# Optimization experiments

Measured on AMD Instinct MI355X. Metric: run time of the kernel, lower is better.

## Reference

```python
import jax, jax.numpy as jnp
import numpy as np

EPS = 1e-3  # eps in grad_pursuit_update_step


def _grad_pursuit(signal, dictionary, target_l0):
    """signal: [B, V], dictionary: [F, V] -> dense weights [B, F] (nonneg)."""
    B, V = signal.shape
    F = dictionary.shape[0]
    rows = jnp.arange(B)

    def step(weights, _):
        # residual = signal - weights @ D         [B, V]
        residual = signal - jnp.einsum('bf,fv->bv', weights, dictionary)
        # inner products with every atom          [B, F]
        inner = jnp.einsum('bv,fv->bf', residual, dictionary)
        idx = jnp.argmax(inner, axis=1)           # [B]
        selected = (weights != 0).at[rows, idx].set(True)
        grad = jnp.where(selected, inner, jnp.zeros((), signal.dtype))  # [B, F]
        c = jnp.einsum('bf,fv->bv', grad, dictionary)                   # [B, V]
        c_sq = jnp.sum(c * c, axis=-1)
        step_size = jnp.sum(c * residual, axis=-1) / jnp.maximum(c_sq, EPS)
        weights = jax.nn.relu(weights + step_size[:, None] * grad)
        return weights, None

    w0 = jnp.zeros((B, F), dtype=signal.dtype)
    weights, _ = jax.lax.scan(step, w0, None, length=target_l0)
    return weights


def _decode(indices, weights, dictionary):
    # embedding-bag sum: gather rows then weighted sum over k
    return jnp.einsum('bk,bkv->bv', weights, dictionary[indices])


def setup_inputs() -> dict:
    key = jax.random.key(0)
    k1, k2, k3, k4, k5 = jax.random.split(key, 5)
    B, D, F = 1024, 1024, 8192
    x = jax.random.normal(k1, (B, D), dtype=jnp.float32)
    y = jax.random.normal(k2, (B, D), dtype=jnp.float32)
    xs = jax.random.normal(k3, (F, D), dtype=jnp.float32)
    xs = xs / jnp.linalg.norm(xs, axis=-1, keepdims=True)  # module stores unit-norm atoms
    ys = jax.random.normal(k4, (F, D), dtype=jnp.float32)
    ys = ys / jnp.linalg.norm(jax.random.normal(k3, (F, D)), axis=-1, keepdims=True)
    mean_y = 0.1 * jax.random.normal(k5, (D,), dtype=jnp.float32)
    return {"x": x, "y": y, "xs": xs, "ys": ys, "mean_y": mean_y, "target_l0": 16}


def reference(x, y, xs, ys, mean_y, target_l0):
    # ITDA.forward with subtract_mean=False, skip_connection=False, fvu_loss=True
    dense = _grad_pursuit(x, xs, target_l0)               # [B, F]
    weights, indices = jax.lax.top_k(dense, target_l0)    # [B, k], [B, k]
    x_rec = _decode(indices, weights, xs)                  # [B, V]
    y_rec = _decode(indices, weights, ys)                  # [B, V]
    l2 = jnp.sum((y - y_rec) ** 2, axis=-1)                # [B]
    total_var = jnp.mean(jnp.sum((y - mean_y) ** 2, axis=-1))
    losses = l2 / total_var
    return weights, indices, x_rec, y_rec, losses
```

## Files before the change

kernel.cpp:

```cpp
#include <hip/hip_runtime.h>
#include <cstdint>
#include <cstddef>

#define B_N 1024
#define V_N 1024
#define F_N 8192
#define NSEL 16
#define NITER 16
#define EPSV 1e-3f
#define WINF 0.008f
#define CANDMAX 64

#define BM 64
#define BN 128
#define BK 32
#define NBN (F_N / BN)

typedef __attribute__((ext_vector_type(4))) float f32x4;
typedef __attribute__((ext_vector_type(8))) short bf16x8;
typedef unsigned short u16;

#define GLDS16(g, l) __builtin_amdgcn_global_load_lds((__attribute__((address_space(1))) void*)(g), (__attribute__((address_space(3))) void*)(l), 16, 0, 0)

__device__ __forceinline__ u16 f2bf(float f) {
  unsigned u = __float_as_uint(f);
  return (u16)((u + 0x7FFFu + ((u >> 16) & 1u)) >> 16);
}

__device__ __forceinline__ float block_sum256(float v, float* sbuf) {
#pragma unroll
  for (int o = 32; o > 0; o >>= 1) v += __shfl_down(v, o, 64);
  int lane = threadIdx.x & 63, wid = threadIdx.x >> 6;
  if (lane == 0) sbuf[wid] = v;
  __syncthreads();
  float r = sbuf[0] + sbuf[1] + sbuf[2] + sbuf[3];
  __syncthreads();
  return r;
}

__device__ __forceinline__ float block_max256(float v, float* sbuf) {
#pragma unroll
  for (int o = 32; o > 0; o >>= 1) v = fmaxf(v, __shfl_down(v, o, 64));
  int lane = threadIdx.x & 63, wid = threadIdx.x >> 6;
  if (lane == 0) sbuf[wid] = v;
  __syncthreads();
  float r = fmaxf(fmaxf(sbuf[0], sbuf[1]), fmaxf(sbuf[2], sbuf[3]));
  __syncthreads();
  return r;
}

__device__ __forceinline__ float seq_dot(const float* __restrict__ xrow,
                                         const float* __restrict__ sr) {
  float acc = 0.f;
  for (int k = 0; k < V_N; k += 4) {
    float4 xv = *(const float4*)(xrow + k);
    acc = __builtin_fmaf(xv.x, sr[k + 0], acc);
    acc = __builtin_fmaf(xv.y, sr[k + 1], acc);
    acc = __builtin_fmaf(xv.z, sr[k + 2], acc);
    acc = __builtin_fmaf(xv.w, sr[k + 3], acc);
  }
  return acc;
}

__global__ __launch_bounds__(256) void rowvar_kernel(const float* __restrict__ y,
                                                     const float* __restrict__ mean_y,
                                                     float* __restrict__ rowvar,
                                                     int* __restrict__ act_cnt) {
  int b = blockIdx.x, t = threadIdx.x;
  __shared__ float sred[4];
  float4 yv = *(const float4*)(y + (size_t)b * V_N + t * 4);
  float4 mv = *(const float4*)(mean_y + t * 4);
  float dx = yv.x - mv.x, dy = yv.y - mv.y, dz = yv.z - mv.z, dw = yv.w - mv.w;
  float p = dx * dx + dy * dy + dz * dz + dw * dw;
  float s = block_sum256(p, sred);
  if (t == 0) { rowvar[b] = s; act_cnt[b] = 0; }
}

__global__ __launch_bounds__(256) void reduce_var_kernel(const float* __restrict__ rowvar,
                                                         float* __restrict__ totvar) {
  __shared__ float sred[4];
  int t = threadIdx.x;
  float p = 0.f;
#pragma unroll
  for (int i = 0; i < 4; i++) p += rowvar[t * 4 + i];
  float s = block_sum256(p, sred);
  if (t == 0) totvar[0] = s / (float)B_N;
}

__global__ __launch_bounds__(256) void xh_kernel(const float* __restrict__ xs,
                                                 u16* __restrict__ Xh) {
  int b = blockIdx.x, t = threadIdx.x;
  float4 v = *(const float4*)(xs + (size_t)b * V_N + t * 4);
  u16* o = Xh + (size_t)b * V_N + t * 4;
  o[0] = f2bf(v.x); o[1] = f2bf(v.y); o[2] = f2bf(v.z); o[3] = f2bf(v.w);
}

__global__ __launch_bounds__(256) void init_kernel(const float* __restrict__ x,
                                                   float* __restrict__ R,
                                                   u16* __restrict__ Rh,
                                                   float* __restrict__ rn2) {
  int b = blockIdx.x, t = threadIdx.x;
  __shared__ float sred[4];
  float4 v = *(const float4*)(x + (size_t)b * V_N + t * 4);
  *(float4*)(R + (size_t)b * V_N + t * 4) = v;
  u16* o = Rh + (size_t)b * V_N + t * 4;
  o[0] = f2bf(v.x); o[1] = f2bf(v.y); o[2] = f2bf(v.z); o[3] = f2bf(v.w);
  float p = v.x * v.x + v.y * v.y + v.z * v.z + v.w * v.w;
  float s = block_sum256(p, sred);
  if (t == 0) rn2[b] = s;
}

__global__ __launch_bounds__(256) void gemm_scan_kernel(const u16* __restrict__ Rh,
                                                        const u16* __restrict__ Xh,
                                                        float* __restrict__ inner) {
  __shared__ u16 As[128 * 32];
  __shared__ u16 Bs[128 * 32];
  const int tid = threadIdx.x;
  const int w = tid >> 6, l = tid & 63;
  const int bn = blockIdx.x, bm = blockIdx.y;
  const int wr = w >> 1, wc = w & 1;
  const int lr = l & 15, lg = l >> 4;

  f32x4 acc[4][4];
#pragma unroll
  for (int m = 0; m < 4; m++)
#pragma unroll
    for (int n = 0; n < 4; n++) acc[m][n] = (f32x4){0.f, 0.f, 0.f, 0.f};

  const u16* Ab = Rh + (size_t)bm * 128 * V_N;
  const u16* Bb = Xh + (size_t)bn * 128 * V_N;
  const int srow = w * 16 + (l >> 2);
  const int scol = (l & 3) * 8;

  for (int k0 = 0; k0 < V_N; k0 += 32) {
#pragma unroll
    for (int i = 0; i < 2; i++) {
      GLDS16(Ab + (size_t)(i * 64 + srow) * V_N + k0 + scol, As + i * 2048 + w * 512);
      GLDS16(Bb + (size_t)(i * 64 + srow) * V_N + k0 + scol, Bs + i * 2048 + w * 512);
    }
    __syncthreads();
    bf16x8 af[4], bfr[4];
#pragma unroll
    for (int m = 0; m < 4; m++) af[m] = *(const bf16x8*)&As[(wr * 64 + m * 16 + lr) * 32 + lg * 8];
#pragma unroll
    for (int n = 0; n < 4; n++) bfr[n] = *(const bf16x8*)&Bs[(wc * 64 + n * 16 + lr) * 32 + lg * 8];
#pragma unroll
    for (int m = 0; m < 4; m++)
#pragma unroll
      for (int n = 0; n < 4; n++)
        acc[m][n] = __builtin_amdgcn_mfma_f32_16x16x32_bf16(af[m], bfr[n], acc[m][n], 0, 0, 0);
    __syncthreads();
  }

#pragma unroll
  for (int m = 0; m < 4; m++) {
    int gm = bm * 128 + wr * 64 + m * 16 + lg * 4;
#pragma unroll
    for (int n = 0; n < 4; n++) {
      int gn = bn * 128 + wc * 64 + n * 16 + lr;
#pragma unroll
      for (int j = 0; j < 4; j++)
        inner[(size_t)(gm + j) * F_N + gn] = acc[m][n][j];
    }
  }
}

__global__ __launch_bounds__(256) void scan_update_kernel(const float* __restrict__ x,
                                                          const float* __restrict__ xs,
                                                          const float* __restrict__ inner,
                                                          float* __restrict__ rn2,
                                                          int* __restrict__ act_ids,
                                                          float* __restrict__ act_w,
                                                          int* __restrict__ act_cnt,
                                                          float* __restrict__ R,
                                                          u16* __restrict__ Rh) {
  int b = blockIdx.x, t = threadIdx.x;
  __shared__ float sr[V_N];
  __shared__ float sred[4];
  __shared__ float smax[4];
  __shared__ int   scand[CANDMAX];
  __shared__ float scval[CANDMAX];
  __shared__ float sfv[256];
  __shared__ int   sfi[256];
  __shared__ int   scnt_c;
  __shared__ int   sbii;
  __shared__ float sg[NSEL + 2];
  __shared__ float sw[NSEL + 2];
  __shared__ int   sids[NSEL + 2];
  __shared__ int   ssel[NSEL + 2];
  __shared__ int   scnt;

  float4 rv = *(const float4*)(R + (size_t)b * V_N + t * 4);
  *(float4*)&sr[t * 4] = rv;
  if (t == 0) scnt_c = 0;
  __syncthreads();

  const float* irow = inner + (size_t)b * F_N;
  float mx = -1e30f;
#pragma unroll
  for (int i = 0; i < 8; i++) {
    float4 v = *(const float4*)&irow[i * 1024 + t * 4];
    mx = fmaxf(mx, fmaxf(fmaxf(v.x, v.y), fmaxf(v.z, v.w)));
  }
  float M = block_max256(mx, smax);
  float win = WINF * sqrtf(rn2[b]);
  float thr = M - win;

#pragma unroll
  for (int i = 0; i < 8; i++) {
    float4 v = *(const float4*)&irow[i * 1024 + t * 4];
    int base = i * 1024 + t * 4;
    if (v.x >= thr) { int p = atomicAdd(&scnt_c, 1); if (p < CANDMAX) scand[p] = base + 0; }
    if (v.y >= thr) { int p = atomicAdd(&scnt_c, 1); if (p < CANDMAX) scand[p] = base + 1; }
    if (v.z >= thr) { int p = atomicAdd(&scnt_c, 1); if (p < CANDMAX) scand[p] = base + 2; }
    if (v.w >= thr) { int p = atomicAdd(&scnt_c, 1); if (p < CANDMAX) scand[p] = base + 3; }
  }
  __syncthreads();
  int total = scnt_c;
  int nc = total < CANDMAX ? total : CANDMAX;

  if (total > CANDMAX) {
    float bv = -1e30f; int bi = 0x7fffffff;
    for (int f = t; f < F_N; f += 256) {
      float acc = seq_dot(xs + (size_t)f * V_N, sr);
      if (acc > bv) { bv = acc; bi = f; }
    }
    sfv[t] = bv; sfi[t] = bi;
    __syncthreads();
    if (t == 0) {
      float bbv = sfv[0]; int bbi = sfi[0];
      for (int c = 1; c < 256; c++) {
        float v = sfv[c]; int id = sfi[c];
        if (v > bbv || (v == bbv && id < bbi)) { bbv = v; bbi = id; }
      }
      sbii = bbi;
    }
  } else if (nc == 1) {
    if (t == 0) sbii = scand[0];
  } else {
    if (t < nc) scval[t] = seq_dot(xs + (size_t)scand[t] * V_N, sr);
    __syncthreads();
    if (t == 0) {
      float bv = scval[0]; int bi = scand[0];
      for (int c = 1; c < nc; c++) {
        float v = scval[c]; int id = scand[c];
        if (v > bv || (v == bv && id < bi)) { bv = v; bi = id; }
      }
      sbii = bi;
    }
  }
  __syncthreads();

  if (t == 0) {
    int bi = sbii;
    int cnt = act_cnt[b];
    for (int j = 0; j < cnt; j++) { sids[j] = act_ids[b * NSEL + j]; sw[j] = act_w[b * NSEL + j]; }
    int pos = -1;
    for (int j = 0; j < cnt; j++) if (sids[j] == bi) pos = j;
    if (pos < 0) { pos = cnt; sids[cnt] = bi; sw[cnt] = 0.f; cnt++; }
    for (int j = 0; j < cnt; j++) ssel[j] = (sw[j] != 0.f) || (j == pos) ? 1 : 0;
    scnt = cnt;
  }
  __syncthreads();
  int cnt = scnt;

  for (int j = 0; j < cnt; j++) {
    if (!ssel[j]) { if (t == 0) sg[j] = 0.f; continue; }
    const float* xr = xs + (size_t)sids[j] * V_N;
    float4 xv = *(const float4*)(xr + t * 4);
    float4 rl = *(const float4*)&sr[t * 4];
    float p = xv.x * rl.x + xv.y * rl.y + xv.z * rl.z + xv.w * rl.w;
    float s = block_sum256(p, sred);
    if (t == 0) sg[j] = s;
  }
  __syncthreads();

  float4 cv = {0.f, 0.f, 0.f, 0.f};
  for (int j = 0; j < cnt; j++) {
    if (ssel[j]) {
      float g = sg[j];
      const float* xr = xs + (size_t)sids[j] * V_N;
      float4 xv = *(const float4*)(xr + t * 4);
      cv.x += g * xv.x; cv.y += g * xv.y; cv.z += g * xv.z; cv.w += g * xv.w;
    }
  }
  float4 rl = *(const float4*)&sr[t * 4];
  float pcsq = cv.x * cv.x + cv.y * cv.y + cv.z * cv.z + cv.w * cv.w;
  float pcr  = cv.x * rl.x + cv.y * rl.y + cv.z * rl.z + cv.w * rl.w;
  float csq = block_sum256(pcsq, sred);
  float cr  = block_sum256(pcr, sred);

  if (t == 0) {
    float step = cr / fmaxf(csq, EPSV);
    for (int j = 0; j < cnt; j++)
      if (ssel[j]) sw[j] = fmaxf(sw[j] + step * sg[j], 0.f);
    for (int j = 0; j < cnt; j++) {
      act_ids[b * NSEL + j] = sids[j];
      act_w[b * NSEL + j] = sw[j];
    }
    act_cnt[b] = cnt;
  }
  __syncthreads();

  float4 r = *(const float4*)(x + (size_t)b * V_N + t * 4);
  for (int j = 0; j < cnt; j++) {
    float wv = sw[j];
    if (wv != 0.f) {
      const float* xr = xs + (size_t)sids[j] * V_N;
      float4 xv = *(const float4*)(xr + t * 4);
      r.x -= wv * xv.x; r.y -= wv * xv.y; r.z -= wv * xv.z; r.w -= wv * xv.w;
    }
  }
  *(float4*)(R + (size_t)b * V_N + t * 4) = r;
  u16* o = Rh + (size_t)b * V_N + t * 4;
  o[0] = f2bf(r.x); o[1] = f2bf(r.y); o[2] = f2bf(r.z); o[3] = f2bf(r.w);
  float p2 = r.x * r.x + r.y * r.y + r.z * r.z + r.w * r.w;
  float s2 = block_sum256(p2, sred);
  if (t == 0) rn2[b] = s2;
}

__global__ __launch_bounds__(256) void residual_kernel(const float* __restrict__ x,
                                                       const float* __restrict__ xs,
                                                       const int* __restrict__ act_ids,
                                                       const float* __restrict__ act_w,
                                                       const int* __restrict__ act_cnt,
                                                       float* __restrict__ R) {
  int b = blockIdx.x, t = threadIdx.x;
  float4 r = *(const float4*)(x + (size_t)b * V_N + t * 4);
  int cnt = act_cnt[b];
  for (int j = 0; j < cnt; j++) {
    float w = act_w[b * NSEL + j];
    if (w != 0.f) {
      const float* xr = xs + (size_t)act_ids[b * NSEL + j] * V_N;
      float4 xv = *(const float4*)(xr + t * 4);
      r.x -= w * xv.x; r.y -= w * xv.y; r.z -= w * xv.z; r.w -= w * xv.w;
    }
  }
  *(float4*)(R + (size_t)b * V_N + t * 4) = r;
}

__global__ __launch_bounds__(256) void gemm_argmax_kernel(const float* __restrict__ R,
                                                          const float* __restrict__ xs,
                                                          float* __restrict__ pval,
                                                          int* __restrict__ pidx) {
  __shared__ float sA[BK * 68];
  __shared__ float sB[BK * 132];
  __shared__ float sMv[64 * 33];
  __shared__ int   sMi[64 * 33];

  int tid = threadIdx.x;
  int bn = blockIdx.x, bm = blockIdx.y;
  float acc[8][4];
#pragma unroll
  for (int i = 0; i < 8; i++)
#pragma unroll
    for (int j = 0; j < 4; j++) acc[i][j] = 0.f;

  int r0 = (tid >> 5) << 3;
  int n0 = (tid & 31) << 2;
  const float* Rbase = R + (size_t)(bm * BM) * V_N;
  const float* Xbase = xs + (size_t)(bn * BN) * V_N;

  for (int k0 = 0; k0 < V_N; k0 += BK) {
    {
      int m = tid >> 2, kf = (tid & 3) * 4;
      float4 v = *(const float4*)(Rbase + (size_t)m * V_N + k0 + kf);
      sA[(kf + 0) * 68 + m] = v.x; sA[(kf + 1) * 68 + m] = v.y;
      sA[(kf + 2) * 68 + m] = v.z; sA[(kf + 3) * 68 + m] = v.w;
      float4 v2 = *(const float4*)(Rbase + (size_t)m * V_N + k0 + kf + 16);
      sA[(kf + 16) * 68 + m] = v2.x; sA[(kf + 17) * 68 + m] = v2.y;
      sA[(kf + 18) * 68 + m] = v2.z; sA[(kf + 19) * 68 + m] = v2.w;
    }
    {
      int nn = tid >> 3, kf = (tid & 7) * 4;
#pragma unroll
      for (int i = 0; i < 4; i++) {
        int n = nn + i * 32;
        float4 v = *(const float4*)(Xbase + (size_t)n * V_N + k0 + kf);
        sB[(kf + 0) * 132 + n] = v.x; sB[(kf + 1) * 132 + n] = v.y;
        sB[(kf + 2) * 132 + n] = v.z; sB[(kf + 3) * 132 + n] = v.w;
      }
    }
    __syncthreads();
#pragma unroll
    for (int k = 0; k < BK; k++) {
      float4 aL = *(float4*)&sA[k * 68 + r0];
      float4 aH = *(float4*)&sA[k * 68 + r0 + 4];
      float4 bv = *(float4*)&sB[k * 132 + n0];
      float a[8] = {aL.x, aL.y, aL.z, aL.w, aH.x, aH.y, aH.z, aH.w};
      float bb[4] = {bv.x, bv.y, bv.z, bv.w};
#pragma unroll
      for (int i = 0; i < 8; i++)
#pragma unroll
        for (int j = 0; j < 4; j++) acc[i][j] += a[i] * bb[j];
    }
    __syncthreads();
  }

#pragma unroll
  for (int i = 0; i < 8; i++) {
    float bvv = acc[i][0]; int bj = 0;
#pragma unroll
    for (int j = 1; j < 4; j++)
      if (acc[i][j] > bvv) { bvv = acc[i][j]; bj = j; }
    sMv[(r0 + i) * 33 + (tid & 31)] = bvv;
    sMi[(r0 + i) * 33 + (tid & 31)] = bn * BN + n0 + bj;
  }
  __syncthreads();
  if (tid < 64) {
    float bvv = sMv[tid * 33]; int bi = sMi[tid * 33];
    for (int c = 1; c < 32; c++) {
      float v = sMv[tid * 33 + c];
      if (v > bvv) { bvv = v; bi = sMi[tid * 33 + c]; }
    }
    pval[(size_t)(bm * BM + tid) * NBN + bn] = bvv;
    pidx[(size_t)(bm * BM + tid) * NBN + bn] = bi;
  }
}

__global__ __launch_bounds__(256) void combine_update_kernel(const float* __restrict__ R,
                                                             const float* __restrict__ xs,
                                                             const float* __restrict__ pval,
                                                             const int* __restrict__ pidx,
                                                             int* __restrict__ act_ids,
                                                             float* __restrict__ act_w,
                                                             int* __restrict__ act_cnt) {
  int b = blockIdx.x, t = threadIdx.x;
  __shared__ float sr[V_N];
  __shared__ float sred[4];
  __shared__ float sg[NSEL + 1];
  __shared__ float sw[NSEL + 1];
  __shared__ int   sids[NSEL + 1];
  __shared__ int   ssel[NSEL + 1];
  __shared__ int   scnt;

  float4 rv = *(const float4*)(R + (size_t)b * V_N + t * 4);
  *(float4*)&sr[t * 4] = rv;

  if (t == 0) {
    const float* pv = pval + (size_t)b * NBN;
    const int* pi = pidx + (size_t)b * NBN;
    float bv = pv[0]; int bi = pi[0];
    for (int c = 1; c < NBN; c++) {
      float v = pv[c];
      if (v > bv) { bv = v; bi = pi[c]; }
    }
    int cnt = act_cnt[b];
    for (int j = 0; j < cnt; j++) { sids[j] = act_ids[b * NSEL + j]; sw[j] = act_w[b * NSEL + j]; }
    int pos = -1;
    for (int j = 0; j < cnt; j++) if (sids[j] == bi) pos = j;
    if (pos < 0) { pos = cnt; sids[cnt] = bi; sw[cnt] = 0.f; cnt++; }
    for (int j = 0; j < cnt; j++) ssel[j] = (sw[j] != 0.f) || (j == pos) ? 1 : 0;
    scnt = cnt;
  }
  __syncthreads();
  int cnt = scnt;

  for (int j = 0; j < cnt; j++) {
    if (!ssel[j]) { if (t == 0) sg[j] = 0.f; continue; }
    const float* xr = xs + (size_t)sids[j] * V_N;
    float4 xv = *(const float4*)(xr + t * 4);
    float4 rl = *(const float4*)&sr[t * 4];
    float p = xv.x * rl.x + xv.y * rl.y + xv.z * rl.z + xv.w * rl.w;
    float s = block_sum256(p, sred);
    if (t == 0) sg[j] = s;
  }
  __syncthreads();

  float4 cv = {0.f, 0.f, 0.f, 0.f};
  for (int j = 0; j < cnt; j++) {
    if (ssel[j]) {
      float g = sg[j];
      const float* xr = xs + (size_t)sids[j] * V_N;
      float4 xv = *(const float4*)(xr + t * 4);
      cv.x += g * xv.x; cv.y += g * xv.y; cv.z += g * xv.z; cv.w += g * xv.w;
    }
  }
  float4 rl = *(const float4*)&sr[t * 4];
  float pcsq = cv.x * cv.x + cv.y * cv.y + cv.z * cv.z + cv.w * cv.w;
  float pcr  = cv.x * rl.x + cv.y * rl.y + cv.z * rl.z + cv.w * rl.w;
  float csq = block_sum256(pcsq, sred);
  float cr  = block_sum256(pcr, sred);

  if (t == 0) {
    float step = cr / fmaxf(csq, EPSV);
    for (int j = 0; j < cnt; j++)
      if (ssel[j]) sw[j] = fmaxf(sw[j] + step * sg[j], 0.f);
    for (int j = 0; j < cnt; j++) {
      act_ids[b * NSEL + j] = sids[j];
      act_w[b * NSEL + j] = sw[j];
    }
    act_cnt[b] = cnt;
  }
}

__global__ __launch_bounds__(256) void topk_kernel(const int* __restrict__ act_ids,
                                                   const float* __restrict__ act_w,
                                                   const int* __restrict__ act_cnt,
                                                   float* __restrict__ out_w,
                                                   float* __restrict__ out_i) {
  int b = blockIdx.x * blockDim.x + threadIdx.x;
  if (b >= B_N) return;
  int cnt = act_cnt[b];
  int ids[NSEL]; float w[NSEL]; int m = 0;
  for (int j = 0; j < cnt; j++) {
    float wv = act_w[b * NSEL + j];
    if (wv > 0.f) { ids[m] = act_ids[b * NSEL + j]; w[m] = wv; m++; }
  }
  for (int i = 1; i < m; i++) {
    float wv = w[i]; int id = ids[i]; int j = i - 1;
    while (j >= 0 && (w[j] < wv || (w[j] == wv && ids[j] > id))) {
      w[j + 1] = w[j]; ids[j + 1] = ids[j]; j--;
    }
    w[j + 1] = wv; ids[j + 1] = id;
  }
  int nf = 0;
  for (int s = m; s < NSEL; s++) {
    for (;;) {
      bool used = false;
      for (int j = 0; j < m; j++) if (ids[j] == nf) used = true;
      if (!used) break;
      nf++;
    }
    ids[s] = nf; w[s] = 0.f; nf++;
  }
  for (int s = 0; s < NSEL; s++) {
    out_w[b * NSEL + s] = w[s];
    out_i[b * NSEL + s] = (float)ids[s];
  }
}

__global__ __launch_bounds__(256) void decode_kernel(const float* __restrict__ y,
                                                     const float* __restrict__ xs,
                                                     const float* __restrict__ ys,
                                                     const float* __restrict__ out_w,
                                                     const float* __restrict__ out_i,
                                                     const float* __restrict__ totvar,
                                                     float* __restrict__ x_rec,
                                                     float* __restrict__ y_rec,
                                                     float* __restrict__ losses) {
  int b = blockIdx.x, t = threadIdx.x;
  __shared__ float swv[NSEL];
  __shared__ int sid[NSEL];
  __shared__ float sred[4];
  if (t < NSEL) { swv[t] = out_w[b * NSEL + t]; sid[t] = (int)out_i[b * NSEL + t]; }
  __syncthreads();
  float4 xr = {0.f, 0.f, 0.f, 0.f}, yr = {0.f, 0.f, 0.f, 0.f};
  for (int s = 0; s < NSEL; s++) {
    float wv = swv[s];
    if (wv != 0.f) {
      const float* xrow = xs + (size_t)sid[s] * V_N;
      const float* yrow = ys + (size_t)sid[s] * V_N;
      float4 a = *(const float4*)(xrow + t * 4);
      float4 c = *(const float4*)(yrow + t * 4);
      xr.x += wv * a.x; xr.y += wv * a.y; xr.z += wv * a.z; xr.w += wv * a.w;
      yr.x += wv * c.x; yr.y += wv * c.y; yr.z += wv * c.z; yr.w += wv * c.w;
    }
  }
  *(float4*)(x_rec + (size_t)b * V_N + t * 4) = xr;
  *(float4*)(y_rec + (size_t)b * V_N + t * 4) = yr;
  float4 yv = *(const float4*)(y + (size_t)b * V_N + t * 4);
  float dx = yv.x - yr.x, dy = yv.y - yr.y, dz = yv.z - yr.z, dw = yv.w - yr.w;
  float p = dx * dx + dy * dy + dz * dz + dw * dw;
  float l2 = block_sum256(p, sred);
  if (t == 0) losses[b] = l2 / totvar[0];
}

extern "C" void kernel_launch(void* const* d_in, const int* in_sizes, int n_in,
                              void* d_out, int out_size, void* d_ws, size_t ws_size,
                              hipStream_t stream) {
  const float* x      = (const float*)d_in[0];
  const float* y      = (const float*)d_in[1];
  const float* xs     = (const float*)d_in[2];
  const float* ys     = (const float*)d_in[3];
  const float* mean_y = (const float*)d_in[4];
  (void)in_sizes; (void)n_in; (void)out_size;

  float* out    = (float*)d_out;
  float* out_w  = out;
  float* out_i  = out + 16384;
  float* out_xr = out + 32768;
  float* out_yr = out + 32768 + 1048576;
  float* out_ls = out + 32768 + 2097152;

  float* ws = (float*)d_ws;

  const size_t FAST_NEED = (size_t)14191617 * 4;

  if (ws_size >= FAST_NEED) {
    float* R     = ws;
    float* inner = ws + 1048576;
    u16*   Rh    = (u16*)(ws + 9437184);
    u16*   Xh    = (u16*)(ws + 9961472);
    float* rn2   = ws + 14155776;
    int*   aid   = (int*)(ws + 14156800);
    float* aw    = ws + 14173184;
    int*   acn   = (int*)(ws + 14189568);
    float* rv    = ws + 14190592;
    float* tv    = ws + 14191616;

    rowvar_kernel<<<B_N, 256, 0, stream>>>(y, mean_y, rv, acn);
    reduce_var_kernel<<<1, 256, 0, stream>>>(rv, tv);
    xh_kernel<<<F_N, 256, 0, stream>>>(xs, Xh);
    init_kernel<<<B_N, 256, 0, stream>>>(x, R, Rh, rn2);

    for (int it = 0; it < NITER; it++) {
      gemm_scan_kernel<<<dim3(F_N / 128, B_N / 128), 256, 0, stream>>>(Rh, Xh, inner);
      scan_update_kernel<<<B_N, 256, 0, stream>>>(x, xs, inner, rn2, aid, aw, acn, R, Rh);
    }

    topk_kernel<<<(B_N + 255) / 256, 256, 0, stream>>>(aid, aw, acn, out_w, out_i);
    decode_kernel<<<B_N, 256, 0, stream>>>(y, xs, ys, out_w, out_i, tv, out_xr, out_yr, out_ls);
  } else {
    float* R    = ws;
    float* pval = ws + 1048576;
    int*   pidx = (int*)(ws + 1114112);
    int*   aid  = (int*)(ws + 1179648);
    float* aw   = ws + 1196032;
    int*   acn  = (int*)(ws + 1212416);
    float* rv   = ws + 1213440;
    float* tv   = ws + 1214464;

    rowvar_kernel<<<B_N, 256, 0, stream>>>(y, mean_y, rv, acn);
    reduce_var_kernel<<<1, 256, 0, stream>>>(rv, tv);

    for (int it = 0; it < NITER; it++) {
      residual_kernel<<<B_N, 256, 0, stream>>>(x, xs, aid, aw, acn, R);
      gemm_argmax_kernel<<<dim3(NBN, B_N / BM), 256, 0, stream>>>(R, xs, pval, pidx);
      combine_update_kernel<<<B_N, 256, 0, stream>>>(R, xs, pval, pidx, aid, aw, acn);
    }

    topk_kernel<<<(B_N + 255) / 256, 256, 0, stream>>>(aid, aw, acn, out_w, out_i);
    decode_kernel<<<B_N, 256, 0, stream>>>(y, xs, ys, out_w, out_i, tv, out_xr, out_yr, out_ls);
  }
}
```

Before: 1.176 ms.

## Fuse per-tile row max into GEMM epilogue and scan only promising tiles

```diff
diff --git a/kernel.cpp b/kernel.cpp
--- a/kernel.cpp
+++ b/kernel.cpp
@@ -10,6 +10,7 @@
 #define EPSV 1e-3f
 #define WINF 0.008f
 #define CANDMAX 64
+#define NTILE 64
 
 #define BM 64
 #define BN 128
@@ -112,9 +113,13 @@
 
 __global__ __launch_bounds__(256) void gemm_scan_kernel(const u16* __restrict__ Rh,
                                                         const u16* __restrict__ Xh,
-                                                        float* __restrict__ inner) {
+                                                        float* __restrict__ inner,
+                                                        float* __restrict__ pval,
+                                                        int* __restrict__ pidx) {
   __shared__ u16 As[128 * 32];
   __shared__ u16 Bs[128 * 32];
+  __shared__ float smv[128 * 32];
+  __shared__ int   smi[128 * 32];
   const int tid = threadIdx.x;
   const int w = tid >> 6, l = tid & 63;
   const int bn = blockIdx.x, bm = blockIdx.y;
@@ -156,18 +161,38 @@
   for (int m = 0; m < 4; m++) {
     int gm = bm * 128 + wr * 64 + m * 16 + lg * 4;
 #pragma unroll
-    for (int n = 0; n < 4; n++) {
-      int gn = bn * 128 + wc * 64 + n * 16 + lr;
-#pragma unroll
-      for (int j = 0; j < 4; j++)
-        inner[(size_t)(gm + j) * F_N + gn] = acc[m][n][j];
-    }
+    for (int j = 0; j < 4; j++) {
+      float bvv = -1e30f; int bj = -1;
+#pragma unroll
+      for (int n = 0; n < 4; n++) {
+        float v = acc[m][n][j];
+        int gn = bn * 128 + wc * 64 + n * 16 + lr;
+        inner[(size_t)(gm + j) * F_N + gn] = v;
+        int col = wc * 64 + n * 16 + lr;
+        if (v > bvv || (v == bvv && col < bj)) { bvv = v; bj = col; }
+      }
+      int row = wr * 64 + m * 16 + lg * 4 + j;
+      smv[row * 32 + wc * 16 + lr] = bvv;
+      smi[row * 32 + wc * 16 + lr] = bj;
+    }
+  }
+  __syncthreads();
+  if (tid < 128) {
+    float bvv = -1e30f; int bi = 0x7fffffff;
+#pragma unroll 4
+    for (int c = 0; c < 32; c++) {
+      float v = smv[tid * 32 + c]; int id = smi[tid * 32 + c];
+      if (v > bvv || (v == bvv && id < bi)) { bvv = v; bi = id; }
+    }
+    pval[(size_t)(bm * 128 + tid) * NTILE + bn] = bvv;
+    pidx[(size_t)(bm * 128 + tid) * NTILE + bn] = bn * 128 + bi;
   }
 }
 
 __global__ __launch_bounds__(256) void scan_update_kernel(const float* __restrict__ x,
                                                           const float* __restrict__ xs,
                                                           const float* __restrict__ inner,
+                                                          const float* __restrict__ pval,
                                                           float* __restrict__ rn2,
                                                           int* __restrict__ act_ids,
                                                           float* __restrict__ act_w,
@@ -176,6 +201,7 @@
                                                           u16* __restrict__ Rh) {
   int b = blockIdx.x, t = threadIdx.x;
   __shared__ float sr[V_N];
+  __shared__ float spv[NTILE];
   __shared__ float sred[4];
   __shared__ float smax[4];
   __shared__ int   scand[CANDMAX];
@@ -192,28 +218,22 @@
 
   float4 rv = *(const float4*)(R + (size_t)b * V_N + t * 4);
   *(float4*)&sr[t * 4] = rv;
+  if (t < NTILE) spv[t] = pval[(size_t)b * NTILE + t];
   if (t == 0) scnt_c = 0;
   __syncthreads();
 
-  const float* irow = inner + (size_t)b * F_N;
-  float mx = -1e30f;
-#pragma unroll
-  for (int i = 0; i < 8; i++) {
-    float4 v = *(const float4*)&irow[i * 1024 + t * 4];
-    mx = fmaxf(mx, fmaxf(fmaxf(v.x, v.y), fmaxf(v.z, v.w)));
-  }
-  float M = block_max256(mx, smax);
+  float M = block_max256(spv[t & (NTILE - 1)], smax);
   float win = WINF * sqrtf(rn2[b]);
   float thr = M - win;
 
-#pragma unroll
-  for (int i = 0; i < 8; i++) {
-    float4 v = *(const float4*)&irow[i * 1024 + t * 4];
-    int base = i * 1024 + t * 4;
-    if (v.x >= thr) { int p = atomicAdd(&scnt_c, 1); if (p < CANDMAX) scand[p] = base + 0; }
-    if (v.y >= thr) { int p = atomicAdd(&scnt_c, 1); if (p < CANDMAX) scand[p] = base + 1; }
-    if (v.z >= thr) { int p = atomicAdd(&scnt_c, 1); if (p < CANDMAX) scand[p] = base + 2; }
-    if (v.w >= thr) { int p = atomicAdd(&scnt_c, 1); if (p < CANDMAX) scand[p] = base + 3; }
+  const float* irow = inner + (size_t)b * F_N;
+  for (int tt = 0; tt < NTILE; tt++) {
+    if (spv[tt] >= thr) {
+      if (t < 128) {
+        float v = irow[tt * 128 + t];
+        if (v >= thr) { int p = atomicAdd(&scnt_c, 1); if (p < CANDMAX) scand[p] = tt * 128 + t; }
+      }
+    }
   }
   __syncthreads();
   int total = scnt_c;
@@ -585,7 +605,7 @@
 
   float* ws = (float*)d_ws;
 
-  const size_t FAST_NEED = (size_t)14191617 * 4;
+  const size_t FAST_NEED = (size_t)14322689 * 4;
 
   if (ws_size >= FAST_NEED) {
     float* R     = ws;
@@ -598,6 +618,8 @@
     int*   acn   = (int*)(ws + 14189568);
     float* rv    = ws + 14190592;
     float* tv    = ws + 14191616;
+    float* pval  = ws + 14191617;
+    int*   pidx  = (int*)(ws + 14257153);
 
     rowvar_kernel<<<B_N, 256, 0, stream>>>(y, mean_y, rv, acn);
     reduce_var_kernel<<<1, 256, 0, stream>>>(rv, tv);
@@ -605,8 +627,8 @@
     init_kernel<<<B_N, 256, 0, stream>>>(x, R, Rh, rn2);
 
     for (int it = 0; it < NITER; it++) {
-      gemm_scan_kernel<<<dim3(F_N / 128, B_N / 128), 256, 0, stream>>>(Rh, Xh, inner);
-      scan_update_kernel<<<B_N, 256, 0, stream>>>(x, xs, inner, rn2, aid, aw, acn, R, Rh);
+      gemm_scan_kernel<<<dim3(F_N / 128, B_N / 128), 256, 0, stream>>>(Rh, Xh, inner, pval, pidx);
+      scan_update_kernel<<<B_N, 256, 0, stream>>>(x, xs, inner, pval, rn2, aid, aw, acn, R, Rh);
     }
 
     topk_kernel<<<(B_N + 255) / 256, 256, 0, stream>>>(aid, aw, acn, out_w, out_i);
```

Result: slower. 1.462 ms (+24.3%).
